# Kernel optimization log

Measured on AMD Instinct MI355X. Metric: run time of the kernel, lower is better.

## Reference

```python
import jax, jax.numpy as jnp
import numpy as np

N_NODES = 100_000
N_EDGES = 1_600_000
N_GRAPHS = 512
NODE_TYPE_BUCKETS = 256
IDENT_BUCKETS = 50_000
NODE_EMB = 64
IDENT_EMB = 32
IN_DIM = NODE_EMB + IDENT_EMB + 6  # 102
HID = 128
NUM_CATS = 10


def setup_inputs() -> dict:
    key = jax.random.key(0)
    ks = jax.random.split(key, 24)
    p = lambda k, shp: (jax.random.normal(k, shp, dtype=jnp.float32) * 0.05)
    return {
        "node_type_ids": jax.random.randint(ks[0], (N_NODES,), 0, NODE_TYPE_BUCKETS + 2),
        "ident_hash_ids": jax.random.randint(ks[1], (N_NODES,), 0, IDENT_BUCKETS + 2),
        "literal_flags": jax.random.uniform(ks[2], (N_NODES, 5), dtype=jnp.float32),
        "node_depth": jax.random.randint(ks[3], (N_NODES,), 0, 60),
        "edge_index": jax.random.randint(ks[4], (2, N_EDGES), 0, N_NODES),
        "batch_index": jnp.sort(jax.random.randint(ks[5], (N_NODES,), 0, N_GRAPHS)),
        "emb_node": p(ks[6], (NODE_TYPE_BUCKETS + 2, NODE_EMB)),
        "emb_ident": p(ks[7], (IDENT_BUCKETS + 2, IDENT_EMB)),
        "W_self0": p(ks[8], (IN_DIM, HID)), "b_self0": p(ks[9], (HID,)),
        "W_neigh0": p(ks[10], (IN_DIM, HID)), "b_neigh0": p(ks[11], (HID,)),
        "W_self1": p(ks[12], (HID, HID)), "b_self1": p(ks[13], (HID,)),
        "W_neigh1": p(ks[14], (HID, HID)), "b_neigh1": p(ks[15], (HID,)),
        "W_risk": p(ks[16], (HID, 1)), "b_risk": p(ks[17], (1,)),
        "W_cat": p(ks[18], (HID, NUM_CATS)), "b_cat": p(ks[19], (NUM_CATS,)),
    }


def reference(node_type_ids, ident_hash_ids, literal_flags, node_depth,
              edge_index, batch_index, emb_node, emb_ident,
              W_self0, b_self0, W_neigh0, b_neigh0,
              W_self1, b_self1, W_neigh1, b_neigh1,
              W_risk, b_risk, W_cat, b_cat):
    n = node_type_ids.shape[0]
    # node features: [N, 64+32+5+1]
    depth = node_depth.astype(jnp.float32)[:, None]
    depth = depth / jnp.maximum(depth.max(), 1.0)
    x = jnp.concatenate([emb_node[node_type_ids], emb_ident[ident_hash_ids],
                         literal_flags, depth], axis=-1)
    src, dst = edge_index[0], edge_index[1]
    # in-degree, shared across layers (clamped to 1)
    deg = jax.ops.segment_sum(jnp.ones_like(dst, jnp.float32), dst, num_segments=n)
    inv_deg = (1.0 / jnp.maximum(deg, 1.0))[:, None]

    def sage(x, Ws, bs, Wn, bn):
        agg = jax.ops.segment_sum(x[src], dst, num_segments=n)  # gather+scatter-sum
        neigh = agg * inv_deg
        return jax.nn.relu(x @ Ws + bs + neigh @ Wn + bn)

    x = sage(x, W_self0, b_self0, W_neigh0, b_neigh0)
    x = sage(x, W_self1, b_self1, W_neigh1, b_neigh1)

    # global mean pool over graphs
    pooled = jax.ops.segment_sum(x, batch_index, num_segments=N_GRAPHS)
    counts = jax.ops.segment_sum(jnp.ones((n,), jnp.float32), batch_index,
                                 num_segments=N_GRAPHS)
    g = pooled / jnp.maximum(counts, 1.0)[:, None]

    risk_logit = (g @ W_risk + b_risk)[:, 0]
    category_logits = g @ W_cat + b_cat
    return risk_logit, category_logits
```

## Files before the change

### kernel.cpp

```cpp
#include <hip/hip_runtime.h>
#include <cstdint>
#include <cstddef>

#define HIDDIM 128
#define NGRAPH_MAX 512
#define LDSPAD 136
#define NBKT_MAX 512


using short8 = __attribute__((ext_vector_type(8))) short;
using f32x4  = __attribute__((ext_vector_type(4))) float;

__device__ __forceinline__ unsigned short f2bf(float x) {
    union { float f; uint32_t u; } v; v.f = x;
    uint32_t r = v.u + 0x7fffu + ((v.u >> 16) & 1u);
    return (unsigned short)(r >> 16);
}
__device__ __forceinline__ uint32_t pack2(float a, float b) {
    return (uint32_t)f2bf(a) | ((uint32_t)f2bf(b) << 16);
}
__device__ __forceinline__ float bflo(uint32_t u) { return __uint_as_float(u << 16); }
__device__ __forceinline__ float bfhi(uint32_t u) { return __uint_as_float(u & 0xffff0000u); }

__global__ void k_prep(const int* __restrict__ nt, const int* __restrict__ ih,
                       const float* __restrict__ flags, const int* __restrict__ depth,
                       const float* __restrict__ embN, const float* __restrict__ embI,
                       const int* __restrict__ edst, const int* __restrict__ batch,
                       const float* __restrict__ Wn0, const float* __restrict__ Ws0,
                       const float* __restrict__ Wn1, const float* __restrict__ Ws1,
                       int K0, int N, int E, int G,
                       unsigned short* __restrict__ x0, unsigned short* __restrict__ Wt,
                       int* __restrict__ bcount, int* __restrict__ counts,
                       int* __restrict__ maxd,
                       int nbF, int nbC, int nbN) {
    __shared__ int hist[NBKT_MAX];
    __shared__ int red[256];
    int b = blockIdx.x, t = threadIdx.x;
    if (b < nbF) {
        int idx = b * 256 + t;
        int i = idx >> 4;
        int seg = idx & 15;
        if (i >= N) return;
        uint4 o = make_uint4(0u, 0u, 0u, 0u);
        if (seg < 8) {
            const float4* r = (const float4*)(embN + (size_t)nt[i] * 64 + seg * 8);
            float4 v0 = r[0], v1 = r[1];
            o.x = pack2(v0.x, v0.y); o.y = pack2(v0.z, v0.w);
            o.z = pack2(v1.x, v1.y); o.w = pack2(v1.z, v1.w);
        } else if (seg < 12) {
            const float4* r = (const float4*)(embI + (size_t)ih[i] * 32 + (seg - 8) * 8);
            float4 v0 = r[0], v1 = r[1];
            o.x = pack2(v0.x, v0.y); o.y = pack2(v0.z, v0.w);
            o.z = pack2(v1.x, v1.y); o.w = pack2(v1.z, v1.w);
        } else if (seg == 12) {
            const float* fp = flags + (size_t)i * 5;
            o.x = pack2(fp[0], fp[1]);
            o.y = pack2(fp[2], fp[3]);
            o.z = pack2(fp[4], 0.f);
        }
        *(uint4*)(x0 + (size_t)i * HIDDIM + seg * 8) = o;
    } else if (b < nbF + nbC) {
        hist[t] = 0; hist[t + 256] = 0;
        __syncthreads();
        int c0 = (b - nbF) * 4096;
        int ce = min(4096, E - c0);
        for (int i = t; i < ce; i += 256)
            atomicAdd(&hist[edst[c0 + i] >> 8], 1);
        __syncthreads();
        for (int bb = t; bb < NBKT_MAX; bb += 256)
            if (hist[bb]) atomicAdd(&bcount[bb], hist[bb]);
    } else if (b < nbF + nbC + nbN) {
        for (int g = t; g < G; g += 256) hist[g] = 0;
        __syncthreads();
        int i = (b - nbF - nbC) * 256 + t;
        int d = 0;
        if (i < N) {
            atomicAdd(&hist[batch[i]], 1);
            d = depth[i];
        }
        red[t] = d;
        __syncthreads();
        for (int off = 128; off > 0; off >>= 1) {
            if (t < off) red[t] = max(red[t], red[t + off]);
            __syncthreads();
        }
        if (t == 0) atomicMax(maxd, red[0]);
        for (int g = t; g < G; g += 256)
            if (hist[g]) atomicAdd(&counts[g], hist[g]);
    } else {
        int idx = (b - nbF - nbC - nbN) * 256 + t;
        int mat = idx >> 14;
        int rem = idx & 16383;
        int n = rem >> 7, k = rem & 127;
        const float* W = (mat == 0) ? Wn0 : (mat == 1) ? Ws0 : (mat == 2) ? Wn1 : Ws1;
        int K = (mat < 2) ? K0 : HIDDIM;
        Wt[(size_t)mat * HIDDIM * HIDDIM + n * HIDDIM + k] =
            (k < K) ? f2bf(W[(size_t)k * HIDDIM + n]) : (unsigned short)0;
    }
}

__global__ void k_bscatter(const int* __restrict__ src, const int* __restrict__ dst,
                           const int* __restrict__ bcount, int* __restrict__ relcnt,
                           uint32_t* __restrict__ ebuf,
                           const int* __restrict__ depth, const int* __restrict__ maxd,
                           unsigned short* __restrict__ x0,
                           int E, int N, int nbkt, int nbC) {
    __shared__ uint32_t stage[4096];
    __shared__ int sbkt[4096];
    __shared__ int hist[NBKT_MAX];
    __shared__ int ofs[NBKT_MAX];
    __shared__ int cur[NBKT_MAX];
    __shared__ int gbase[NBKT_MAX];
    __shared__ int boffL[NBKT_MAX];
    __shared__ int scanbuf[256];
    int b = blockIdx.x, t = threadIdx.x;

    if (b >= nbC) {
        int i = (b - nbC) * 256 + t;
        if (i < N) {
            float md = fmaxf((float)(*maxd), 1.0f);
            x0[(size_t)i * HIDDIM + 101] = f2bf((float)depth[i] / md);
        }
        return;
    }

    {
        int e0 = 2 * t, e1 = 2 * t + 1;
        int v0 = (e0 < nbkt) ? bcount[e0] : 0;
        int v1 = (e1 < nbkt) ? bcount[e1] : 0;
        int ps = v0 + v1;
        scanbuf[t] = ps;
        __syncthreads();
        for (int off = 1; off < 256; off <<= 1) {
            int x = (t >= off) ? scanbuf[t - off] : 0;
            __syncthreads();
            scanbuf[t] += x;
            __syncthreads();
        }
        int ex = scanbuf[t] - ps;
        boffL[e0] = ex;
        boffL[e1] = ex + v0;
    }
    __syncthreads();

    int c0 = b * 4096;
    int ce = min(4096, E - c0);
    hist[t] = 0; hist[t + 256] = 0;
    __syncthreads();
    for (int i = t; i < ce; i += 256)
        atomicAdd(&hist[dst[c0 + i] >> 8], 1);
    __syncthreads();
    int h2a = hist[2 * t], h2b = hist[2 * t + 1];
    int ps = h2a + h2b;
    scanbuf[t] = ps;
    __syncthreads();
    for (int off = 1; off < 256; off <<= 1) {
        int x = (t >= off) ? scanbuf[t - off] : 0;
        __syncthreads();
        scanbuf[t] += x;
        __syncthreads();
    }
    int ex = scanbuf[t] - ps;
    ofs[2 * t] = ex;           cur[2 * t] = ex;
    ofs[2 * t + 1] = ex + h2a; cur[2 * t + 1] = ex + h2a;
    __syncthreads();
    for (int i = t; i < ce; i += 256) {
        int d = dst[c0 + i];
        int p = atomicAdd(&cur[d >> 8], 1);
        stage[p] = (uint32_t)src[c0 + i] | ((uint32_t)(d & 255) << 24);
        sbkt[p] = d >> 8;
    }
    __syncthreads();
    for (int bb = t; bb < nbkt; bb += 256) {
        int c = hist[bb];
        gbase[bb] = c ? (boffL[bb] + atomicAdd(&relcnt[bb], c)) : 0;
    }
    __syncthreads();
    for (int j = t; j < ce; j += 256) {
        int bk = sbkt[j];
        ebuf[gbase[bk] + (j - ofs[bk])] = stage[j];
    }
}

__global__ void k_build(const uint32_t* __restrict__ ebuf, const int* __restrict__ bcount,
                        int* __restrict__ rowptr, float* __restrict__ invd,
                        int* __restrict__ srcs, int N, int E, int nbkt) {
    __shared__ int ldeg[256];
    __shared__ int lofs[256];
    __shared__ int lcur[256];
    __shared__ int boffL[NBKT_MAX + 1];
    __shared__ int scanbuf[256];
    int b = blockIdx.x, t = threadIdx.x;

    {
        int e0 = 2 * t, e1 = 2 * t + 1;
        int v0 = (e0 < nbkt) ? bcount[e0] : 0;
        int v1 = (e1 < nbkt) ? bcount[e1] : 0;
        int ps = v0 + v1;
        scanbuf[t] = ps;
        __syncthreads();
        for (int off = 1; off < 256; off <<= 1) {
            int x = (t >= off) ? scanbuf[t - off] : 0;
            __syncthreads();
            scanbuf[t] += x;
            __syncthreads();
        }
        int ex = scanbuf[t] - ps;
        boffL[e0] = ex;
        boffL[e1] = ex + v0;
        if (t == 255) boffL[512] = scanbuf[255];
    }
    __syncthreads();

    int n0 = b << 8;
    int s = boffL[b], e = boffL[b + 1];
    if (b == 0 && t == 0) rowptr[N] = E;
    ldeg[t] = 0;
    __syncthreads();
    for (int i = s + t; i < e; i += 256)
        atomicAdd(&ldeg[ebuf[i] >> 24], 1);
    __syncthreads();
    int v = ldeg[t];
    lofs[t] = v;
    __syncthreads();
    for (int off = 1; off < 256; off <<= 1) {
        int x = (t >= off) ? lofs[t - off] : 0;
        __syncthreads();
        lofs[t] += x;
        __syncthreads();
    }
    int excl = lofs[t] - v;
    int node = n0 + t;
    if (node < N) {
        rowptr[node] = s + excl;
        invd[node] = 1.0f / (float)max(v, 1);
    }
    lcur[t] = excl;
    __syncthreads();
    for (int i = s + t; i < e; i += 256) {
        uint32_t p = ebuf[i];
        int slot = atomicAdd(&lcur[p >> 24], 1);
        srcs[s + slot] = (int)(p & 0x00FFFFFFu);
    }
}

__global__ void k_aggc(const uint4* __restrict__ x4, const int* __restrict__ rp,
                       const int* __restrict__ srcs, const float* __restrict__ invd,
                       uint4* __restrict__ axo, int N) {
    int t = threadIdx.x;
    int lane = t & 63;
    int q = lane >> 4;
    int cl = lane & 15;
    int d = blockIdx.x * 4 + (t >> 6);
    if (d >= N) return;
    int s = rp[d], e = rp[d + 1];
    float a0 = 0.f, a1 = 0.f, a2 = 0.f, a3 = 0.f,
          a4 = 0.f, a5 = 0.f, a6 = 0.f, a7 = 0.f;
#define ACC8(u) { a0 += bflo(u.x); a1 += bfhi(u.x); a2 += bflo(u.y); a3 += bfhi(u.y); \
                  a4 += bflo(u.z); a5 += bfhi(u.z); a6 += bflo(u.w); a7 += bfhi(u.w); }
    for (int base = s; base < e; base += 64) {
        int m = min(64, e - base);
        int idx = (lane < m) ? srcs[base + lane] : 0;
        int j = 0;
        for (; j + 16 <= m; j += 16) {
            int i0 = __shfl(idx, j + q, 64);
            int i1 = __shfl(idx, j + 4 + q, 64);
            int i2 = __shfl(idx, j + 8 + q, 64);
            int i3 = __shfl(idx, j + 12 + q, 64);
            uint4 u0 = x4[(size_t)i0 * 16 + cl];
            uint4 u1 = x4[(size_t)i1 * 16 + cl];
            uint4 u2 = x4[(size_t)i2 * 16 + cl];
            uint4 u3 = x4[(size_t)i3 * 16 + cl];
            ACC8(u0); ACC8(u1); ACC8(u2); ACC8(u3);
        }
        for (; j + 4 <= m; j += 4) {
            int id = __shfl(idx, j + q, 64);
            uint4 u = x4[(size_t)id * 16 + cl];
            ACC8(u);
        }
        if (j < m) {
            int id = __shfl(idx, min(j + q, m - 1), 64);
            if (q < m - j) {
                uint4 u = x4[(size_t)id * 16 + cl];
                ACC8(u);
            }
        }
    }
#undef ACC8
    a0 += __shfl_down(a0, 32, 64); a1 += __shfl_down(a1, 32, 64);
    a2 += __shfl_down(a2, 32, 64); a3 += __shfl_down(a3, 32, 64);
    a4 += __shfl_down(a4, 32, 64); a5 += __shfl_down(a5, 32, 64);
    a6 += __shfl_down(a6, 32, 64); a7 += __shfl_down(a7, 32, 64);
    a0 += __shfl_down(a0, 16, 64); a1 += __shfl_down(a1, 16, 64);
    a2 += __shfl_down(a2, 16, 64); a3 += __shfl_down(a3, 16, 64);
    a4 += __shfl_down(a4, 16, 64); a5 += __shfl_down(a5, 16, 64);
    a6 += __shfl_down(a6, 16, 64); a7 += __shfl_down(a7, 16, 64);
    if (q == 0) {
        float iv = invd[d];
        uint4 o;
        o.x = pack2(a0 * iv, a1 * iv);
        o.y = pack2(a2 * iv, a3 * iv);
        o.z = pack2(a4 * iv, a5 * iv);
        o.w = pack2(a6 * iv, a7 * iv);
        axo[(size_t)d * 16 + cl] = o;
    }
}

__global__ __launch_bounds__(256, 2) void k_gemm3(
    const unsigned short* __restrict__ X, const unsigned short* __restrict__ AX,
    const unsigned short* __restrict__ Wts, const unsigned short* __restrict__ Wtn,
    int N, const float* __restrict__ bias_s, const float* __restrict__ bias_n,
    unsigned short* __restrict__ Xo) {
    __shared__ unsigned short Bs[128 * LDSPAD];
    __shared__ unsigned short Bn[128 * LDSPAD];
    int t = threadIdx.x;
    int rowBase = blockIdx.x << 7;

    #pragma unroll
    for (int it = 0; it < 8; it++) {
        int idx = t + it * 256;
        int n = idx >> 4, seg = idx & 15;
        *(uint4*)&Bs[n * LDSPAD + seg * 8] = *(const uint4*)(Wts + n * HIDDIM + seg * 8);
        *(uint4*)&Bn[n * LDSPAD + seg * 8] = *(const uint4*)(Wtn + n * HIDDIM + seg * 8);
    }

    int lane = t & 63;
    int wv = t >> 6;
    int ml = lane & 15;
    int quad = lane >> 4;
    int m0 = wv * 32;

    const uint4* X4 = (const uint4*)X;
    const uint4* A4 = (const uint4*)AX;
    int gr0 = rowBase + m0 + ml;
    int gr1 = gr0 + 16;
    uint4 fx0[4], fx1[4], fa0[4], fa1[4];
    #pragma unroll
    for (int kt = 0; kt < 4; kt++) {
        uint4 z = make_uint4(0u, 0u, 0u, 0u);
        size_t o0 = (size_t)gr0 * 16 + kt * 4 + quad;
        size_t o1 = (size_t)gr1 * 16 + kt * 4 + quad;
        fx0[kt] = (gr0 < N) ? X4[o0] : z;
        fx1[kt] = (gr1 < N) ? X4[o1] : z;
        fa0[kt] = (gr0 < N) ? A4[o0] : z;
        fa1[kt] = (gr1 < N) ? A4[o1] : z;
    }
    __syncthreads();

    f32x4 acc[2][8];
    #pragma unroll
    for (int i = 0; i < 2; i++)
        #pragma unroll
        for (int j = 0; j < 8; j++) acc[i][j] = (f32x4){0.f, 0.f, 0.f, 0.f};

    #pragma unroll
    for (int kt = 0; kt < 4; kt++) {
        int ko = kt * 32 + quad * 8;
        short8 x0f = *(short8*)&fx0[kt];
        short8 x1f = *(short8*)&fx1[kt];
        short8 a0f = *(short8*)&fa0[kt];
        short8 a1f = *(short8*)&fa1[kt];
        #pragma unroll
        for (int nt = 0; nt < 8; nt++) {
            short8 bs = *(const short8*)&Bs[(nt * 16 + ml) * LDSPAD + ko];
            short8 bn = *(const short8*)&Bn[(nt * 16 + ml) * LDSPAD + ko];
            acc[0][nt] = __builtin_amdgcn_mfma_f32_16x16x32_bf16(x0f, bs, acc[0][nt], 0, 0, 0);
            acc[1][nt] = __builtin_amdgcn_mfma_f32_16x16x32_bf16(x1f, bs, acc[1][nt], 0, 0, 0);
            acc[0][nt] = __builtin_amdgcn_mfma_f32_16x16x32_bf16(a0f, bn, acc[0][nt], 0, 0, 0);
            acc[1][nt] = __builtin_amdgcn_mfma_f32_16x16x32_bf16(a1f, bn, acc[1][nt], 0, 0, 0);
        }
    }

    float bsum[8];
    #pragma unroll
    for (int nt = 0; nt < 8; nt++) {
        int col = nt * 16 + ml;
        bsum[nt] = bias_s[col] + bias_n[col];
    }

    __syncthreads();
    #pragma unroll
    for (int mt = 0; mt < 2; mt++) {
        int lrow0 = m0 + mt * 16 + quad * 4;
        #pragma unroll
        for (int r = 0; r < 4; r++)
            #pragma unroll
            for (int nt = 0; nt < 8; nt++)
                Bs[(lrow0 + r) * LDSPAD + nt * 16 + ml] =
                    f2bf(fmaxf(acc[mt][nt][r] + bsum[nt], 0.f));
    }
    __syncthreads();
    #pragma unroll
    for (int it = 0; it < 8; it++) {
        int idx = t + it * 256;
        int r = idx >> 4, seg = idx & 15;
        int gr = rowBase + r;
        if (gr < N)
            *(uint4*)(Xo + (size_t)gr * HIDDIM + seg * 8) = *(const uint4*)&Bs[r * LDSPAD + seg * 8];
    }
}

__global__ void k_poolhead(const uint32_t* __restrict__ x, const int* __restrict__ counts,
                           const float* __restrict__ Wr, const float* __restrict__ br,
                           const float* __restrict__ Wc, const float* __restrict__ bc,
                           float* __restrict__ out, int G) {
    __shared__ float red[3][128];
    __shared__ float rowf[128];
    __shared__ int gexcl[NGRAPH_MAX + 1];
    __shared__ int scanbuf[256];
    int gr = blockIdx.x, t = threadIdx.x;

    {
        int e0 = 2 * t, e1 = 2 * t + 1;
        int v0 = (e0 < G) ? counts[e0] : 0;
        int v1 = (e1 < G) ? counts[e1] : 0;
        int ps = v0 + v1;
        scanbuf[t] = ps;
        __syncthreads();
        for (int off = 1; off < 256; off <<= 1) {
            int x2 = (t >= off) ? scanbuf[t - off] : 0;
            __syncthreads();
            scanbuf[t] += x2;
            __syncthreads();
        }
        int ex = scanbuf[t] - ps;
        gexcl[e0] = ex;
        gexcl[e1] = ex + v0;
        if (t == 255) gexcl[512] = scanbuf[255];
    }
    __syncthreads();

    int wv = t >> 6, lane = t & 63;
    int half = lane >> 5, cl = lane & 31;
    int s = gexcl[gr], e = gexcl[gr + 1];
    const uint2* x2p = (const uint2*)x;
    float a0 = 0.f, a1 = 0.f, a2 = 0.f, a3 = 0.f;
    for (int r0 = s + wv * 2 + half; r0 < e; r0 += 32) {
        uint2 u0 = x2p[(size_t)r0 * 32 + cl];
        int r1 = r0 + 8, r2 = r0 + 16, r3 = r0 + 24;
        uint2 u1 = make_uint2(0u, 0u), u2 = make_uint2(0u, 0u), u3 = make_uint2(0u, 0u);
        if (r1 < e) u1 = x2p[(size_t)r1 * 32 + cl];
        if (r2 < e) u2 = x2p[(size_t)r2 * 32 + cl];
        if (r3 < e) u3 = x2p[(size_t)r3 * 32 + cl];
        a0 += bflo(u0.x); a1 += bfhi(u0.x); a2 += bflo(u0.y); a3 += bfhi(u0.y);
        a0 += bflo(u1.x); a1 += bfhi(u1.x); a2 += bflo(u1.y); a3 += bfhi(u1.y);
        a0 += bflo(u2.x); a1 += bfhi(u2.x); a2 += bflo(u2.y); a3 += bfhi(u2.y);
        a0 += bflo(u3.x); a1 += bfhi(u3.x); a2 += bflo(u3.y); a3 += bfhi(u3.y);
    }
    a0 += __shfl_down(a0, 32, 64);
    a1 += __shfl_down(a1, 32, 64);
    a2 += __shfl_down(a2, 32, 64);
    a3 += __shfl_down(a3, 32, 64);
    if (half == 0 && wv > 0) {
        red[wv - 1][cl * 4 + 0] = a0;
        red[wv - 1][cl * 4 + 1] = a1;
        red[wv - 1][cl * 4 + 2] = a2;
        red[wv - 1][cl * 4 + 3] = a3;
    }
    __syncthreads();
    if (wv == 0 && half == 0) {
        a0 += red[0][cl * 4 + 0] + red[1][cl * 4 + 0] + red[2][cl * 4 + 0];
        a1 += red[0][cl * 4 + 1] + red[1][cl * 4 + 1] + red[2][cl * 4 + 1];
        a2 += red[0][cl * 4 + 2] + red[1][cl * 4 + 2] + red[2][cl * 4 + 2];
        a3 += red[0][cl * 4 + 3] + red[1][cl * 4 + 3] + red[2][cl * 4 + 3];
        float inv = 1.0f / fmaxf((float)counts[gr], 1.0f);
        rowf[cl * 4 + 0] = a0 * inv;
        rowf[cl * 4 + 1] = a1 * inv;
        rowf[cl * 4 + 2] = a2 * inv;
        rowf[cl * 4 + 3] = a3 * inv;
    }
    __syncthreads();
    if (t == 0) {
        float s2 = 0.f;
        for (int k = 0; k < 128; k++) s2 += rowf[k] * Wr[k];
        out[gr] = s2 + br[0];
    } else if (t <= 10) {
        int j = t - 1;
        float s2 = 0.f;
        for (int k = 0; k < 128; k++) s2 += rowf[k] * Wc[k * 10 + j];
        out[G + gr * 10 + j] = s2 + bc[j];
    }
}

extern "C" void kernel_launch(void* const* d_in, const int* in_sizes, int n_in,
                              void* d_out, int out_size, void* d_ws, size_t ws_size,
                              hipStream_t stream) {
    const int*   nt    = (const int*)d_in[0];
    const int*   ih    = (const int*)d_in[1];
    const float* flags = (const float*)d_in[2];
    const int*   depth = (const int*)d_in[3];
    const int*   eidx  = (const int*)d_in[4];
    const int*   batch = (const int*)d_in[5];
    const float* embN  = (const float*)d_in[6];
    const float* embI  = (const float*)d_in[7];
    const float* Ws0   = (const float*)d_in[8];
    const float* bs0   = (const float*)d_in[9];
    const float* Wn0   = (const float*)d_in[10];
    const float* bn0   = (const float*)d_in[11];
    const float* Ws1   = (const float*)d_in[12];
    const float* bs1   = (const float*)d_in[13];
    const float* Wn1   = (const float*)d_in[14];
    const float* bn1   = (const float*)d_in[15];
    const float* Wr    = (const float*)d_in[16];
    const float* br    = (const float*)d_in[17];
    const float* Wc    = (const float*)d_in[18];
    const float* bc    = (const float*)d_in[19];
    float* out = (float*)d_out;

    const int N  = in_sizes[0];
    const int E  = in_sizes[4] / 2;
    const int K0 = in_sizes[8] / HIDDIM;
    const int G  = out_size / 11;
    const int* esrc = eidx;
    const int* edst = eidx + E;
    const int NBKT = (N + 255) >> 8;

    char* w = (char*)d_ws;
    const size_t NH = (size_t)N * HIDDIM * sizeof(unsigned short);
    unsigned short* bufA  = (unsigned short*)(w);
    unsigned short* bufB  = (unsigned short*)(w + NH);
    unsigned short* bufAX = (unsigned short*)(w + 2 * NH);
    char* p = w + 3 * NH;
    unsigned short* Wt = (unsigned short*)p; p += (size_t)4 * HIDDIM * HIDDIM * 2;
    uint32_t* ebuf = (uint32_t*)p;   p += (size_t)E * 4;
    int* srcs   = (int*)p;           p += (size_t)E * 4;
    int* rowptr = (int*)p;           p += (size_t)(N + 1) * 4;
    float* invd = (float*)p;         p += (size_t)N * 4;
    int* relcnt = (int*)p;           p += (size_t)NBKT_MAX * 4;
    int* bcount = (int*)p;           p += (size_t)NBKT_MAX * 4;
    int* counts = (int*)p;           p += (size_t)G * 4;
    int* maxd   = (int*)p;           p += 4;
    const size_t zero_bytes = (size_t)(2 * NBKT_MAX + G + 1) * 4;
    (void)n_in; (void)ws_size;

    const int nbC = (E + 4095) / 4096;
    const int nbN = (N + 255) / 256;
    const int nbF = ((size_t)N * 16 + 255) / 256;
    const int nbG2 = (N + 127) / 128;
    const int nbA = (N + 3) / 4;

    hipMemsetAsync(relcnt, 0, zero_bytes, stream);

    k_prep<<<nbF + nbC + nbN + 256, 256, 0, stream>>>(
        nt, ih, flags, depth, embN, embI, edst, batch,
        Wn0, Ws0, Wn1, Ws1, K0, N, E, G,
        bufA, Wt, bcount, counts, maxd, nbF, nbC, nbN);

    k_bscatter<<<nbC + nbN, 256, 0, stream>>>(esrc, edst, bcount, relcnt, ebuf,
                                              depth, maxd, bufA, E, N, NBKT, nbC);
    k_build<<<NBKT, 256, 0, stream>>>(ebuf, bcount, rowptr, invd, srcs, N, E, NBKT);

    const unsigned short* Wt_n0 = Wt;
    const unsigned short* Wt_s0 = Wt + 1 * HIDDIM * HIDDIM;
    const unsigned short* Wt_n1 = Wt + 2 * HIDDIM * HIDDIM;
    const unsigned short* Wt_s1 = Wt + 3 * HIDDIM * HIDDIM;

    k_aggc<<<nbA, 256, 0, stream>>>((const uint4*)bufA, rowptr, srcs, invd,
                                    (uint4*)bufAX, N);
    k_gemm3<<<nbG2, 256, 0, stream>>>(bufA, bufAX, Wt_s0, Wt_n0, N, bs0, bn0, bufB);

    k_aggc<<<nbA, 256, 0, stream>>>((const uint4*)bufB, rowptr, srcs, invd,
                                    (uint4*)bufAX, N);
    k_gemm3<<<nbG2, 256, 0, stream>>>(bufB, bufAX, Wt_s1, Wt_n1, N, bs1, bn1, bufA);

    k_poolhead<<<G, 256, 0, stream>>>((const uint32_t*)bufA, counts,
                                      Wr, br, Wc, bc, out, G);
}
```

Measured before the change: 340.2 us.

## Fuse neighbor aggregation into the SAGE layer GEMM kernel via LDS

The separate gather-aggregate kernel and the dual-GEMM kernel are merged into one per-layer kernel. Each 128-row block first aggregates its rows' neighbor features into LDS, then runs the self GEMM and the neighbor GEMM, reusing one LDS weight buffer for both. This removes the global write and re-read of the aggregated buffer and one launch per layer. In exchange each block's gather phase is serialized (32 rows per wave), grid parallelism during aggregation falls from 25k blocks to 782, and latency hiding depends on two blocks per CU.

```diff
diff --git a/kernel.cpp b/kernel.cpp
--- a/kernel.cpp
+++ b/kernel.cpp
@@ -244,108 +244,101 @@
     }
 }
 
-__global__ void k_aggc(const uint4* __restrict__ x4, const int* __restrict__ rp,
-                       const int* __restrict__ srcs, const float* __restrict__ invd,
-                       uint4* __restrict__ axo, int N) {
+__global__ __launch_bounds__(256, 2) void k_lay(
+    const unsigned short* __restrict__ X,
+    const unsigned short* __restrict__ Wts, const unsigned short* __restrict__ Wtn,
+    const int* __restrict__ rp, const int* __restrict__ srcs,
+    const float* __restrict__ invd,
+    int N, const float* __restrict__ bias_s, const float* __restrict__ bias_n,
+    unsigned short* __restrict__ Xo) {
+    __shared__ unsigned short axs[128 * LDSPAD];
+    __shared__ unsigned short Bw[128 * LDSPAD];
     int t = threadIdx.x;
+    int rowBase = blockIdx.x << 7;
     int lane = t & 63;
+    int wv = t >> 6;
     int q = lane >> 4;
     int cl = lane & 15;
-    int d = blockIdx.x * 4 + (t >> 6);
-    if (d >= N) return;
-    int s = rp[d], e = rp[d + 1];
-    float a0 = 0.f, a1 = 0.f, a2 = 0.f, a3 = 0.f,
-          a4 = 0.f, a5 = 0.f, a6 = 0.f, a7 = 0.f;
-#define ACC8(u) { a0 += bflo(u.x); a1 += bfhi(u.x); a2 += bflo(u.y); a3 += bfhi(u.y); \
-                  a4 += bflo(u.z); a5 += bfhi(u.z); a6 += bflo(u.w); a7 += bfhi(u.w); }
-    for (int base = s; base < e; base += 64) {
-        int m = min(64, e - base);
-        int idx = (lane < m) ? srcs[base + lane] : 0;
-        int j = 0;
-        for (; j + 16 <= m; j += 16) {
-            int i0 = __shfl(idx, j + q, 64);
-            int i1 = __shfl(idx, j + 4 + q, 64);
-            int i2 = __shfl(idx, j + 8 + q, 64);
-            int i3 = __shfl(idx, j + 12 + q, 64);
-            uint4 u0 = x4[(size_t)i0 * 16 + cl];
-            uint4 u1 = x4[(size_t)i1 * 16 + cl];
-            uint4 u2 = x4[(size_t)i2 * 16 + cl];
-            uint4 u3 = x4[(size_t)i3 * 16 + cl];
-            ACC8(u0); ACC8(u1); ACC8(u2); ACC8(u3);
-        }
-        for (; j + 4 <= m; j += 4) {
-            int id = __shfl(idx, j + q, 64);
-            uint4 u = x4[(size_t)id * 16 + cl];
-            ACC8(u);
-        }
-        if (j < m) {
-            int id = __shfl(idx, min(j + q, m - 1), 64);
-            if (q < m - j) {
-                uint4 u = x4[(size_t)id * 16 + cl];
-                ACC8(u);
-            }
-        }
-    }
-#undef ACC8
-    a0 += __shfl_down(a0, 32, 64); a1 += __shfl_down(a1, 32, 64);
-    a2 += __shfl_down(a2, 32, 64); a3 += __shfl_down(a3, 32, 64);
-    a4 += __shfl_down(a4, 32, 64); a5 += __shfl_down(a5, 32, 64);
-    a6 += __shfl_down(a6, 32, 64); a7 += __shfl_down(a7, 32, 64);
-    a0 += __shfl_down(a0, 16, 64); a1 += __shfl_down(a1, 16, 64);
-    a2 += __shfl_down(a2, 16, 64); a3 += __shfl_down(a3, 16, 64);
-    a4 += __shfl_down(a4, 16, 64); a5 += __shfl_down(a5, 16, 64);
-    a6 += __shfl_down(a6, 16, 64); a7 += __shfl_down(a7, 16, 64);
-    if (q == 0) {
-        float iv = invd[d];
-        uint4 o;
-        o.x = pack2(a0 * iv, a1 * iv);
-        o.y = pack2(a2 * iv, a3 * iv);
-        o.z = pack2(a4 * iv, a5 * iv);
-        o.w = pack2(a6 * iv, a7 * iv);
-        axo[(size_t)d * 16 + cl] = o;
-    }
-}
-
-__global__ __launch_bounds__(256, 2) void k_gemm3(
-    const unsigned short* __restrict__ X, const unsigned short* __restrict__ AX,
-    const unsigned short* __restrict__ Wts, const unsigned short* __restrict__ Wtn,
-    int N, const float* __restrict__ bias_s, const float* __restrict__ bias_n,
-    unsigned short* __restrict__ Xo) {
-    __shared__ unsigned short Bs[128 * LDSPAD];
-    __shared__ unsigned short Bn[128 * LDSPAD];
-    int t = threadIdx.x;
-    int rowBase = blockIdx.x << 7;
 
     #pragma unroll
     for (int it = 0; it < 8; it++) {
         int idx = t + it * 256;
         int n = idx >> 4, seg = idx & 15;
-        *(uint4*)&Bs[n * LDSPAD + seg * 8] = *(const uint4*)(Wts + n * HIDDIM + seg * 8);
-        *(uint4*)&Bn[n * LDSPAD + seg * 8] = *(const uint4*)(Wtn + n * HIDDIM + seg * 8);
-    }
-
-    int lane = t & 63;
-    int wv = t >> 6;
+        *(uint4*)&Bw[n * LDSPAD + seg * 8] = *(const uint4*)(Wts + n * HIDDIM + seg * 8);
+    }
+
+    const uint4* x4 = (const uint4*)X;
+    for (int rr = 0; rr < 32; rr++) {
+        int lr = rr * 4 + wv;
+        int d = rowBase + lr;
+        float a0 = 0.f, a1 = 0.f, a2 = 0.f, a3 = 0.f,
+              a4 = 0.f, a5 = 0.f, a6 = 0.f, a7 = 0.f;
+        if (d < N) {
+            int s = rp[d], e = rp[d + 1];
+#define ACC8(u) { a0 += bflo(u.x); a1 += bfhi(u.x); a2 += bflo(u.y); a3 += bfhi(u.y); \
+                  a4 += bflo(u.z); a5 += bfhi(u.z); a6 += bflo(u.w); a7 += bfhi(u.w); }
+            for (int base = s; base < e; base += 64) {
+                int m = min(64, e - base);
+                int idx = (lane < m) ? srcs[base + lane] : 0;
+                int j = 0;
+                for (; j + 16 <= m; j += 16) {
+                    int i0 = __shfl(idx, j + q, 64);
+                    int i1 = __shfl(idx, j + 4 + q, 64);
+                    int i2 = __shfl(idx, j + 8 + q, 64);
+                    int i3 = __shfl(idx, j + 12 + q, 64);
+                    uint4 u0 = x4[(size_t)i0 * 16 + cl];
+                    uint4 u1 = x4[(size_t)i1 * 16 + cl];
+                    uint4 u2 = x4[(size_t)i2 * 16 + cl];
+                    uint4 u3 = x4[(size_t)i3 * 16 + cl];
+                    ACC8(u0); ACC8(u1); ACC8(u2); ACC8(u3);
+                }
+                for (; j + 4 <= m; j += 4) {
+                    int id = __shfl(idx, j + q, 64);
+                    uint4 u = x4[(size_t)id * 16 + cl];
+                    ACC8(u);
+                }
+                if (j < m) {
+                    int id = __shfl(idx, min(j + q, m - 1), 64);
+                    if (q < m - j) {
+                        uint4 u = x4[(size_t)id * 16 + cl];
+                        ACC8(u);
+                    }
+                }
+            }
+#undef ACC8
+        }
+        a0 += __shfl_down(a0, 32, 64); a1 += __shfl_down(a1, 32, 64);
+        a2 += __shfl_down(a2, 32, 64); a3 += __shfl_down(a3, 32, 64);
+        a4 += __shfl_down(a4, 32, 64); a5 += __shfl_down(a5, 32, 64);
+        a6 += __shfl_down(a6, 32, 64); a7 += __shfl_down(a7, 32, 64);
+        a0 += __shfl_down(a0, 16, 64); a1 += __shfl_down(a1, 16, 64);
+        a2 += __shfl_down(a2, 16, 64); a3 += __shfl_down(a3, 16, 64);
+        a4 += __shfl_down(a4, 16, 64); a5 += __shfl_down(a5, 16, 64);
+        a6 += __shfl_down(a6, 16, 64); a7 += __shfl_down(a7, 16, 64);
+        if (q == 0) {
+            float iv = (d < N) ? invd[d] : 0.f;
+            uint4 o;
+            o.x = pack2(a0 * iv, a1 * iv);
+            o.y = pack2(a2 * iv, a3 * iv);
+            o.z = pack2(a4 * iv, a5 * iv);
+            o.w = pack2(a6 * iv, a7 * iv);
+            *(uint4*)&axs[lr * LDSPAD + cl * 8] = o;
+        }
+    }
+    __syncthreads();
+
     int ml = lane & 15;
     int quad = lane >> 4;
     int m0 = wv * 32;
-
-    const uint4* X4 = (const uint4*)X;
-    const uint4* A4 = (const uint4*)AX;
     int gr0 = rowBase + m0 + ml;
     int gr1 = gr0 + 16;
-    uint4 fx0[4], fx1[4], fa0[4], fa1[4];
+    uint4 fx0[4], fx1[4];
     #pragma unroll
     for (int kt = 0; kt < 4; kt++) {
         uint4 z = make_uint4(0u, 0u, 0u, 0u);
-        size_t o0 = (size_t)gr0 * 16 + kt * 4 + quad;
-        size_t o1 = (size_t)gr1 * 16 + kt * 4 + quad;
-        fx0[kt] = (gr0 < N) ? X4[o0] : z;
-        fx1[kt] = (gr1 < N) ? X4[o1] : z;
-        fa0[kt] = (gr0 < N) ? A4[o0] : z;
-        fa1[kt] = (gr1 < N) ? A4[o1] : z;
-    }
-    __syncthreads();
+        fx0[kt] = (gr0 < N) ? ((const uint4*)X)[(size_t)gr0 * 16 + kt * 4 + quad] : z;
+        fx1[kt] = (gr1 < N) ? ((const uint4*)X)[(size_t)gr1 * 16 + kt * 4 + quad] : z;
+    }
 
     f32x4 acc[2][8];
     #pragma unroll
@@ -358,14 +351,31 @@
         int ko = kt * 32 + quad * 8;
         short8 x0f = *(short8*)&fx0[kt];
         short8 x1f = *(short8*)&fx1[kt];
-        short8 a0f = *(short8*)&fa0[kt];
-        short8 a1f = *(short8*)&fa1[kt];
         #pragma unroll
         for (int nt = 0; nt < 8; nt++) {
-            short8 bs = *(const short8*)&Bs[(nt * 16 + ml) * LDSPAD + ko];
-            short8 bn = *(const short8*)&Bn[(nt * 16 + ml) * LDSPAD + ko];
+            short8 bs = *(const short8*)&Bw[(nt * 16 + ml) * LDSPAD + ko];
             acc[0][nt] = __builtin_amdgcn_mfma_f32_16x16x32_bf16(x0f, bs, acc[0][nt], 0, 0, 0);
             acc[1][nt] = __builtin_amdgcn_mfma_f32_16x16x32_bf16(x1f, bs, acc[1][nt], 0, 0, 0);
+        }
+    }
+    __syncthreads();
+
+    #pragma unroll
+    for (int it = 0; it < 8; it++) {
+        int idx = t + it * 256;
+        int n = idx >> 4, seg = idx & 15;
+        *(uint4*)&Bw[n * LDSPAD + seg * 8] = *(const uint4*)(Wtn + n * HIDDIM + seg * 8);
+    }
+    __syncthreads();
+
+    #pragma unroll
+    for (int kt = 0; kt < 4; kt++) {
+        int ko = kt * 32 + quad * 8;
+        short8 a0f = *(const short8*)&axs[(m0 + ml) * LDSPAD + ko];
+        short8 a1f = *(const short8*)&axs[(m0 + 16 + ml) * LDSPAD + ko];
+        #pragma unroll
+        for (int nt = 0; nt < 8; nt++) {
+            short8 bn = *(const short8*)&Bw[(nt * 16 + ml) * LDSPAD + ko];
             acc[0][nt] = __builtin_amdgcn_mfma_f32_16x16x32_bf16(a0f, bn, acc[0][nt], 0, 0, 0);
             acc[1][nt] = __builtin_amdgcn_mfma_f32_16x16x32_bf16(a1f, bn, acc[1][nt], 0, 0, 0);
         }
@@ -386,7 +396,7 @@
         for (int r = 0; r < 4; r++)
             #pragma unroll
             for (int nt = 0; nt < 8; nt++)
-                Bs[(lrow0 + r) * LDSPAD + nt * 16 + ml] =
+                axs[(lrow0 + r) * LDSPAD + nt * 16 + ml] =
                     f2bf(fmaxf(acc[mt][nt][r] + bsum[nt], 0.f));
     }
     __syncthreads();
@@ -396,7 +406,7 @@
         int r = idx >> 4, seg = idx & 15;
         int gr = rowBase + r;
         if (gr < N)
-            *(uint4*)(Xo + (size_t)gr * HIDDIM + seg * 8) = *(const uint4*)&Bs[r * LDSPAD + seg * 8];
+            *(uint4*)(Xo + (size_t)gr * HIDDIM + seg * 8) = *(const uint4*)&axs[r * LDSPAD + seg * 8];
     }
 }
 
@@ -519,8 +529,7 @@
     const size_t NH = (size_t)N * HIDDIM * sizeof(unsigned short);
     unsigned short* bufA  = (unsigned short*)(w);
     unsigned short* bufB  = (unsigned short*)(w + NH);
-    unsigned short* bufAX = (unsigned short*)(w + 2 * NH);
-    char* p = w + 3 * NH;
+    char* p = w + 2 * NH;
     unsigned short* Wt = (unsigned short*)p; p += (size_t)4 * HIDDIM * HIDDIM * 2;
     uint32_t* ebuf = (uint32_t*)p;   p += (size_t)E * 4;
     int* srcs   = (int*)p;           p += (size_t)E * 4;
@@ -537,7 +546,6 @@
     const int nbN = (N + 255) / 256;
     const int nbF = ((size_t)N * 16 + 255) / 256;
     const int nbG2 = (N + 127) / 128;
-    const int nbA = (N + 3) / 4;
 
     hipMemsetAsync(relcnt, 0, zero_bytes, stream);
 
@@ -555,13 +563,10 @@
     const unsigned short* Wt_n1 = Wt + 2 * HIDDIM * HIDDIM;
     const unsigned short* Wt_s1 = Wt + 3 * HIDDIM * HIDDIM;
 
-    k_aggc<<<nbA, 256, 0, stream>>>((const uint4*)bufA, rowptr, srcs, invd,
-                                    (uint4*)bufAX, N);
-    k_gemm3<<<nbG2, 256, 0, stream>>>(bufA, bufAX, Wt_s0, Wt_n0, N, bs0, bn0, bufB);
-
-    k_aggc<<<nbA, 256, 0, stream>>>((const uint4*)bufB, rowptr, srcs, invd,
-                                    (uint4*)bufAX, N);
-    k_gemm3<<<nbG2, 256, 0, stream>>>(bufB, bufAX, Wt_s1, Wt_n1, N, bs1, bn1, bufA);
+    k_lay<<<nbG2, 256, 0, stream>>>(bufA, Wt_s0, Wt_n0, rowptr, srcs, invd,
+                                    N, bs0, bn0, bufB);
+    k_lay<<<nbG2, 256, 0, stream>>>(bufB, Wt_s1, Wt_n1, rowptr, srcs, invd,
+                                    N, bs1, bn1, bufA);
 
     k_poolhead<<<G, 256, 0, stream>>>((const uint32_t*)bufA, counts,
                                       Wr, br, Wc, bc, out, G);
```

Result: slower. 514.8 us (+51.3%).
